# Optimization experiments

Hardware: AMD Instinct MI355X
Metric: run time of the kernel (lower is better)

Reference implementation:

```python
import jax, jax.numpy as jnp
import numpy as np

NUM_HEADS = 8

def setup_inputs() -> dict:
    key = jax.random.key(0)
    ks = jax.random.split(key, 4)
    S, B, E, ENC = 2048, 4, 512, 32
    def xavier(k, shape):
        fan_in, fan_out = shape[1], shape[0]
        lim = float(np.sqrt(6.0 / (fan_in + fan_out)))
        return jax.random.uniform(k, shape, jnp.float32, -lim, lim)
    return {
        "query": jax.random.normal(ks[0], (S, B, E), jnp.float32),
        "in_proj_weight": xavier(ks[1], (2 * ENC, E)),
        "in_proj_bias": jnp.zeros((2 * ENC,), jnp.float32),
        "v_proj_weight": xavier(ks[2], (E, E)),
        "v_proj_bias": jnp.zeros((E,), jnp.float32),
        "out_proj_weight": xavier(ks[3], (E, E)),
        "out_proj_bias": jnp.zeros((E,), jnp.float32),
    }

def reference(query, in_proj_weight, in_proj_bias, v_proj_weight, v_proj_bias,
              out_proj_weight, out_proj_bias):
    S, B, E = query.shape
    H = NUM_HEADS
    qk = query @ in_proj_weight.T + in_proj_bias          # [S, B, 2*ENC]
    q, k = jnp.split(qk, 2, axis=-1)                      # [S, B, ENC] each
    v = query @ v_proj_weight.T + v_proj_bias             # [S, B, E]
    ENC = q.shape[-1]
    dq = ENC // H   # q/k head dim (small, e.g. 4)
    dv = E // H     # v head dim (e.g. 64)
    scaling = dq ** -0.5
    # [S,B,H,d] -> [B,H,S,d]; torch's view(S, B*H, d) flattens b-major, h-minor
    q = (q * scaling).reshape(S, B, H, dq).transpose(1, 2, 0, 3)
    k = k.reshape(S, B, H, dq).transpose(1, 2, 0, 3)
    v = v.reshape(S, B, H, dv).transpose(1, 2, 0, 3)
    scores = jnp.einsum('bhsd,bhtd->bhst', q, k)          # [B,H,S,S]
    attn = jax.nn.softmax(scores, axis=-1)
    out = jnp.einsum('bhst,bhtd->bhsd', attn, v)          # [B,H,S,dv]
    out = out.transpose(2, 0, 1, 3).reshape(S, B, E)
    out = out @ out_proj_weight.T + out_proj_bias
    avg_weights = attn.sum(axis=1) / H                    # [B,S,S]
    return out, avg_weights
```

## Files before the change

### kernel.cpp

```cpp
#include <hip/hip_runtime.h>
#include <hip/hip_bf16.h>

#define S_LEN 2048
#define B_SZ 4
#define E_DIM 512
#define H_NUM 8
#define DQ 4
#define DV 64

typedef __attribute__((ext_vector_type(8))) short s16x8;
typedef __attribute__((ext_vector_type(4))) float f32x4;
typedef unsigned short u16;

__device__ __forceinline__ u16 f2b(float x) {
    __hip_bfloat16 h = __float2bfloat16(x);
    return *(u16*)&h;
}

__global__ __launch_bounds__(256) void cast_bf16(
    const float* __restrict__ q,  u16* __restrict__ qb,
    const float* __restrict__ w1, u16* __restrict__ w1b,
    const float* __restrict__ w2, u16* __restrict__ w2b,
    const float* __restrict__ w3, u16* __restrict__ w3b)
{
    const int NQ = S_LEN * B_SZ * E_DIM / 8;
    const int N1 = 64 * E_DIM / 8;
    const int N2 = E_DIM * E_DIM / 8;
    const int total = NQ + N1 + 2 * N2;
    for (int g = blockIdx.x * 256 + threadIdx.x; g < total; g += gridDim.x * 256) {
        const float* src; u16* dst; int off;
        if (g < NQ)                { src = q;  dst = qb;  off = g; }
        else if (g < NQ + N1)      { src = w1; dst = w1b; off = g - NQ; }
        else if (g < NQ + N1 + N2) { src = w2; dst = w2b; off = g - NQ - N1; }
        else                       { src = w3; dst = w3b; off = g - NQ - N1 - N2; }
        float4 a = ((const float4*)src)[(size_t)off * 2];
        float4 b = ((const float4*)src)[(size_t)off * 2 + 1];
        s16x8 o;
        o[0] = f2b(a.x); o[1] = f2b(a.y); o[2] = f2b(a.z); o[3] = f2b(a.w);
        o[4] = f2b(b.x); o[5] = f2b(b.y); o[6] = f2b(b.z); o[7] = f2b(b.w);
        ((s16x8*)dst)[off] = o;
    }
}

template <int MODE>
__global__ __launch_bounds__(256) void gemm_mfma(
    const u16* __restrict__ Abf,
    const u16* __restrict__ W1, const float* __restrict__ b1,
    const u16* __restrict__ W2, const float* __restrict__ b2,
    float* __restrict__ C,
    float* __restrict__ qs, float* __restrict__ ks,
    u16* __restrict__ vsb,
    int N, int K)
{
    constexpr int PP = 72;
    __shared__ __align__(16) u16 As[128][PP];
    __shared__ __align__(16) u16 Bs[64][PP];

    const int m0 = blockIdx.x * 128;
    const int n0 = blockIdx.y * 64;
    const int tid = threadIdx.x;
    const int w = tid >> 6, lane = tid & 63;
    const int wm = w >> 1, wn = w & 1;
    const int fr = lane & 15;
    const int fk = (lane >> 4) << 3;

    const u16* Wsel; int nbase;
    if (MODE == 0 || n0 < 64) { Wsel = W1; nbase = n0; }
    else                      { Wsel = W2; nbase = n0 - 64; }

    const int ar = tid >> 1, ah = (tid & 1) << 5;
    const int br = tid >> 2, bq = (tid & 3) << 4;

    f32x4 acc[4][2];
#pragma unroll
    for (int mt = 0; mt < 4; ++mt)
#pragma unroll
        for (int nt = 0; nt < 2; ++nt) acc[mt][nt] = (f32x4){0.f, 0.f, 0.f, 0.f};

    for (int kp = 0; kp < K; kp += 64) {
        const s16x8* ap = (const s16x8*)&Abf[(size_t)(m0 + ar) * K + kp + ah];
        s16x8 a0 = ap[0], a1 = ap[1], a2 = ap[2], a3 = ap[3];
        const s16x8* bp = (const s16x8*)&Wsel[(size_t)(nbase + br) * K + kp + bq];
        s16x8 b0 = bp[0], b1v = bp[1];
        __syncthreads();
        *(s16x8*)&As[ar][ah + 0]  = a0;
        *(s16x8*)&As[ar][ah + 8]  = a1;
        *(s16x8*)&As[ar][ah + 16] = a2;
        *(s16x8*)&As[ar][ah + 24] = a3;
        *(s16x8*)&Bs[br][bq + 0]  = b0;
        *(s16x8*)&Bs[br][bq + 8]  = b1v;
        __syncthreads();

#pragma unroll
        for (int kb = 0; kb < 2; ++kb) {
            s16x8 bf0 = *(const s16x8*)&Bs[wn * 32 + fr][(kb << 5) + fk];
            s16x8 bf1 = *(const s16x8*)&Bs[wn * 32 + 16 + fr][(kb << 5) + fk];
#pragma unroll
            for (int mt = 0; mt < 4; ++mt) {
                s16x8 af = *(const s16x8*)&As[wm * 64 + mt * 16 + fr][(kb << 5) + fk];
                acc[mt][0] = __builtin_amdgcn_mfma_f32_16x16x32_bf16(af, bf0, acc[mt][0], 0, 0, 0);
                acc[mt][1] = __builtin_amdgcn_mfma_f32_16x16x32_bf16(af, bf1, acc[mt][1], 0, 0, 0);
            }
        }
    }

#pragma unroll
    for (int mt = 0; mt < 4; ++mt)
#pragma unroll
        for (int nt = 0; nt < 2; ++nt)
#pragma unroll
            for (int j = 0; j < 4; ++j) {
                int m = m0 + wm * 64 + mt * 16 + ((lane >> 4) << 2) + j;
                int c = n0 + wn * 32 + nt * 16 + fr;
                float val = acc[mt][nt][j];
                if (MODE == 0) {
                    C[(size_t)m * N + c] = val + b1[c];
                } else {
                    int s  = m >> 2;
                    int bb = m & 3;
                    if (c < 64) {
                        val += b1[c];
                        if (c < 32) {
                            qs[((((size_t)bb * H_NUM) + (c >> 2)) * S_LEN + s) * DQ + (c & 3)] = val * 0.5f;
                        } else {
                            int j2 = c - 32;
                            ks[((((size_t)bb * H_NUM) + (j2 >> 2)) * S_LEN + s) * DQ + (j2 & 3)] = val;
                        }
                    } else {
                        int j2 = c - 64;
                        val += b2[j2];
                        vsb[((((size_t)bb * H_NUM) + (j2 >> 6)) * S_LEN + s) * DV + (j2 & 63)] = f2b(val);
                    }
                }
            }
}

__global__ __launch_bounds__(256) void lsum_kernel(
    const float* __restrict__ qs, const float* __restrict__ ks,
    float* __restrict__ linv)
{
    const int bh = blockIdx.x;
    const int s0 = blockIdx.y * 64;
    const int sl = threadIdx.x >> 2;
    const int tq = threadIdx.x & 3;
    __shared__ float Ksm[S_LEN][DQ];
    __shared__ float part[64][4];
    const float* kp = ks + (size_t)bh * S_LEN * DQ;
    for (int i = threadIdx.x; i < S_LEN; i += 256)
        *(float4*)&Ksm[i][0] = *(const float4*)&kp[(size_t)i * DQ];
    __syncthreads();

    const float4 q = *(const float4*)&qs[((size_t)bh * S_LEN + s0 + sl) * DQ];
    float l = 0.f;
    const int t0 = tq * (S_LEN / 4);
#pragma unroll 4
    for (int t = t0; t < t0 + S_LEN / 4; ++t) {
        float4 kk = *(const float4*)&Ksm[t][0];
        float sc = q.x * kk.x + q.y * kk.y + q.z * kk.z + q.w * kk.w;
        l += __expf(sc);
    }
    part[sl][tq] = l;
    __syncthreads();
    if (threadIdx.x < 64) {
        float tsum = part[threadIdx.x][0] + part[threadIdx.x][1] +
                     part[threadIdx.x][2] + part[threadIdx.x][3];
        linv[(size_t)bh * S_LEN + s0 + threadIdx.x] = 1.0f / tsum;
    }
}

__global__ __launch_bounds__(512) void attn_fused(
    const float* __restrict__ qs, const float* __restrict__ ks,
    const u16* __restrict__ vsb, const float* __restrict__ linv,
    float* __restrict__ aw, u16* __restrict__ ao)
{
    constexpr int TQ = 32, TT = 64, PP = 72;
    const int b = blockIdx.x;
    const int s0 = blockIdx.y * TQ;
    const int tid = threadIdx.x;
    const int w = tid >> 6;
    const int lane = tid & 63;

    __shared__ float Kc[H_NUM][TT][DQ];
    __shared__ float qt[H_NUM][TQ][DQ];
    __shared__ float linvs[H_NUM][TQ];
    __shared__ __align__(16) u16 pb[H_NUM][TQ][PP];
    __shared__ __align__(16) u16 vt[H_NUM][DV][PP];

    if (tid < 256) {
        int h = tid >> 5, s = tid & 31;
        *(float4*)&qt[h][s][0] =
            *(const float4*)&qs[((((size_t)b * H_NUM) + h) * S_LEN + s0 + s) * DQ];
        linvs[h][s] = linv[(((size_t)b * H_NUM) + h) * S_LEN + s0 + s];
    }

    f32x4 acc[2][4];
#pragma unroll
    for (int m = 0; m < 2; ++m)
#pragma unroll
        for (int n = 0; n < 4; ++n) acc[m][n] = (f32x4){0.f, 0.f, 0.f, 0.f};

    const u16* vb = vsb + (((size_t)b * H_NUM) + w) * S_LEN * DV;
    const float* krow = ks + (((size_t)b * H_NUM) + w) * S_LEN * DQ;
    float* awrow = aw + ((size_t)b * S_LEN + s0) * S_LEN;

    const int fr = lane & 15;
    const int fk = (lane >> 4) << 3;

    for (int t0 = 0; t0 < S_LEN; t0 += TT) {
        __syncthreads();

        *(float4*)&Kc[w][lane][0] = *(const float4*)&krow[(size_t)(t0 + lane) * DQ];
        {
            const u16* vrow = vb + (size_t)(t0 + lane) * DV;
#pragma unroll
            for (int g = 0; g < 8; ++g) {
                s16x8 vv = *(const s16x8*)(vrow + (g << 3));
#pragma unroll
                for (int j = 0; j < 8; ++j)
                    vt[w][(g << 3) + j][lane] = (u16)vv[j];
            }
        }
        __syncthreads();

        float awacc[4] = {0.f, 0.f, 0.f, 0.f};
        for (int h = 0; h < H_NUM; ++h) {
            float4 kk = *(const float4*)&Kc[h][lane][0];
#pragma unroll
            for (int it = 0; it < 4; ++it) {
                int s = w + (it << 3);
                float4 q = *(const float4*)&qt[h][s][0];
                float sc = q.x * kk.x + q.y * kk.y + q.z * kk.z + q.w * kk.w;
                float p = __expf(sc) * linvs[h][s];
                pb[h][s][lane] = f2b(p);
                awacc[it] += p;
            }
        }
#pragma unroll
        for (int it = 0; it < 4; ++it)
            awrow[(size_t)(w + (it << 3)) * S_LEN + t0 + lane] = awacc[it] * 0.125f;

        __syncthreads();

#pragma unroll
        for (int kb = 0; kb < 2; ++kb) {
            s16x8 a0 = *(const s16x8*)&pb[w][fr][(kb << 5) + fk];
            s16x8 a1 = *(const s16x8*)&pb[w][16 + fr][(kb << 5) + fk];
#pragma unroll
            for (int n = 0; n < 4; ++n) {
                s16x8 bb = *(const s16x8*)&vt[w][(n << 4) + fr][(kb << 5) + fk];
                acc[0][n] = __builtin_amdgcn_mfma_f32_16x16x32_bf16(a0, bb, acc[0][n], 0, 0, 0);
                acc[1][n] = __builtin_amdgcn_mfma_f32_16x16x32_bf16(a1, bb, acc[1][n], 0, 0, 0);
            }
        }
    }

#pragma unroll
    for (int m = 0; m < 2; ++m)
#pragma unroll
        for (int n = 0; n < 4; ++n)
#pragma unroll
            for (int j = 0; j < 4; ++j) {
                int s = (m << 4) + ((lane >> 4) << 2) + j;
                int d = (n << 4) + (lane & 15);
                ao[((size_t)(s0 + s) * B_SZ + b) * E_DIM + (w * DV + d)] =
                    f2b(acc[m][n][j]);
            }
}

extern "C" void kernel_launch(void* const* d_in, const int* in_sizes, int n_in,
                              void* d_out, int out_size, void* d_ws, size_t ws_size,
                              hipStream_t stream) {
    const float* query = (const float*)d_in[0];
    const float* ipw   = (const float*)d_in[1];
    const float* ipb   = (const float*)d_in[2];
    const float* vpw   = (const float*)d_in[3];
    const float* vpb   = (const float*)d_in[4];
    const float* opw   = (const float*)d_in[5];
    const float* opb   = (const float*)d_in[6];

    float* out_main = (float*)d_out;
    float* aw       = (float*)d_out + (size_t)S_LEN * B_SZ * E_DIM;

    const size_t NQKV = (size_t)B_SZ * H_NUM * S_LEN;
    float* qs   = (float*)d_ws;
    float* ks   = qs + NQKV * DQ;
    float* linv = ks + NQKV * DQ;
    u16* vsb    = (u16*)(linv + NQKV);
    u16* qbf    = vsb + (size_t)S_LEN * B_SZ * E_DIM;
    u16* aobf   = qbf;
    u16* ipwbf  = qbf + (size_t)S_LEN * B_SZ * E_DIM;
    u16* vpwbf  = ipwbf + 64 * E_DIM;
    u16* opwbf  = vpwbf + (size_t)E_DIM * E_DIM;

    cast_bf16<<<1024, 256, 0, stream>>>(query, qbf, ipw, ipwbf, vpw, vpwbf, opw, opwbf);

    dim3 g1(8192 / 128, 576 / 64);
    gemm_mfma<1><<<g1, 256, 0, stream>>>(qbf, ipwbf, ipb, vpwbf, vpb,
                                         nullptr, qs, ks, vsb, 576, E_DIM);

    lsum_kernel<<<dim3(B_SZ * H_NUM, S_LEN / 64), 256, 0, stream>>>(qs, ks, linv);

    attn_fused<<<dim3(B_SZ, S_LEN / 32), 512, 0, stream>>>(qs, ks, vsb, linv, aw, aobf);

    dim3 g4(8192 / 128, 512 / 64);
    gemm_mfma<0><<<g4, 256, 0, stream>>>(aobf, opwbf, opb, nullptr, nullptr,
                                         out_main, nullptr, nullptr, nullptr, E_DIM, E_DIM);
}
```

Baseline: 328.5 us.

## Store V transposed in global memory and recompute probabilities in MFMA fragments

The QKV projection now writes V transposed ([b,h,d,s]), so the attention kernel loads V tiles with vector copies instead of a scalar per-element transpose into shared memory. The bf16 probability tile in shared memory is gone. Each wave recomputes the exp scores for its own head directly into its MFMA A fragments, which removes one barrier per tile. The costs are duplicated exp work and strided 2-byte scatter stores in the GEMM epilogue when writing transposed V.

Result: slower. 362.6 us (+10.4%).

```diff
diff --git a/kernel.cpp b/kernel.cpp
--- a/kernel.cpp
+++ b/kernel.cpp
@@ -49,7 +49,7 @@
     const u16* __restrict__ W2, const float* __restrict__ b2,
     float* __restrict__ C,
     float* __restrict__ qs, float* __restrict__ ks,
-    u16* __restrict__ vsb,
+    u16* __restrict__ vtg,
     int N, int K)
 {
     constexpr int PP = 72;
@@ -129,7 +129,7 @@
                     } else {
                         int j2 = c - 64;
                         val += b2[j2];
-                        vsb[((((size_t)bb * H_NUM) + (j2 >> 6)) * S_LEN + s) * DV + (j2 & 63)] = f2b(val);
+                        vtg[((((size_t)bb * H_NUM) + (j2 >> 6)) * DV + (j2 & 63)) * S_LEN + s] = f2b(val);
                     }
                 }
             }
@@ -170,7 +170,7 @@
 
 __global__ __launch_bounds__(512) void attn_fused(
     const float* __restrict__ qs, const float* __restrict__ ks,
-    const u16* __restrict__ vsb, const float* __restrict__ linv,
+    const u16* __restrict__ vtg, const float* __restrict__ linv,
     float* __restrict__ aw, u16* __restrict__ ao)
 {
     constexpr int TQ = 32, TT = 64, PP = 72;
@@ -183,7 +183,6 @@
     __shared__ float Kc[H_NUM][TT][DQ];
     __shared__ float qt[H_NUM][TQ][DQ];
     __shared__ float linvs[H_NUM][TQ];
-    __shared__ __align__(16) u16 pb[H_NUM][TQ][PP];
     __shared__ __align__(16) u16 vt[H_NUM][DV][PP];
 
     if (tid < 256) {
@@ -192,59 +191,67 @@
             *(const float4*)&qs[((((size_t)b * H_NUM) + h) * S_LEN + s0 + s) * DQ];
         linvs[h][s] = linv[(((size_t)b * H_NUM) + h) * S_LEN + s0 + s];
     }
-
-    f32x4 acc[2][4];
-#pragma unroll
-    for (int m = 0; m < 2; ++m)
-#pragma unroll
-        for (int n = 0; n < 4; ++n) acc[m][n] = (f32x4){0.f, 0.f, 0.f, 0.f};
-
-    const u16* vb = vsb + (((size_t)b * H_NUM) + w) * S_LEN * DV;
-    const float* krow = ks + (((size_t)b * H_NUM) + w) * S_LEN * DQ;
-    float* awrow = aw + ((size_t)b * S_LEN + s0) * S_LEN;
+    __syncthreads();
 
     const int fr = lane & 15;
     const int fk = (lane >> 4) << 3;
 
+    float lr[H_NUM][4];
+#pragma unroll
+    for (int h = 0; h < H_NUM; ++h)
+#pragma unroll
+        for (int it = 0; it < 4; ++it) lr[h][it] = linvs[h][w + (it << 3)];
+    float4 qA0 = *(const float4*)&qt[w][fr][0];
+    float4 qA1 = *(const float4*)&qt[w][16 + fr][0];
+    float lv0 = linvs[w][fr], lv1 = linvs[w][16 + fr];
+
+    f32x4 acc[2][4];
+#pragma unroll
+    for (int m = 0; m < 2; ++m)
+#pragma unroll
+        for (int n = 0; n < 4; ++n) acc[m][n] = (f32x4){0.f, 0.f, 0.f, 0.f};
+
+    const float* krow = ks + (((size_t)b * H_NUM) + w) * S_LEN * DQ;
+    const u16* vrow = vtg + ((((size_t)b * H_NUM) + w) * DV + lane) * S_LEN;
+    float* awrow = aw + ((size_t)b * S_LEN + s0) * S_LEN;
+
     for (int t0 = 0; t0 < S_LEN; t0 += TT) {
         __syncthreads();
 
         *(float4*)&Kc[w][lane][0] = *(const float4*)&krow[(size_t)(t0 + lane) * DQ];
-        {
-            const u16* vrow = vb + (size_t)(t0 + lane) * DV;
-#pragma unroll
-            for (int g = 0; g < 8; ++g) {
-                s16x8 vv = *(const s16x8*)(vrow + (g << 3));
-#pragma unroll
-                for (int j = 0; j < 8; ++j)
-                    vt[w][(g << 3) + j][lane] = (u16)vv[j];
-            }
+#pragma unroll
+        for (int i = 0; i < 8; ++i) {
+            s16x8 vv = *(const s16x8*)(vrow + t0 + (i << 3));
+            *(s16x8*)&vt[w][lane][i << 3] = vv;
         }
         __syncthreads();
 
         float awacc[4] = {0.f, 0.f, 0.f, 0.f};
+#pragma unroll 2
         for (int h = 0; h < H_NUM; ++h) {
             float4 kk = *(const float4*)&Kc[h][lane][0];
 #pragma unroll
             for (int it = 0; it < 4; ++it) {
-                int s = w + (it << 3);
-                float4 q = *(const float4*)&qt[h][s][0];
+                float4 q = *(const float4*)&qt[h][w + (it << 3)][0];
                 float sc = q.x * kk.x + q.y * kk.y + q.z * kk.z + q.w * kk.w;
-                float p = __expf(sc) * linvs[h][s];
-                pb[h][s][lane] = f2b(p);
-                awacc[it] += p;
+                awacc[it] += __expf(sc) * lr[h][it];
             }
         }
 #pragma unroll
         for (int it = 0; it < 4; ++it)
             awrow[(size_t)(w + (it << 3)) * S_LEN + t0 + lane] = awacc[it] * 0.125f;
 
-        __syncthreads();
-
 #pragma unroll
         for (int kb = 0; kb < 2; ++kb) {
-            s16x8 a0 = *(const s16x8*)&pb[w][fr][(kb << 5) + fk];
-            s16x8 a1 = *(const s16x8*)&pb[w][16 + fr][(kb << 5) + fk];
+            s16x8 a0, a1;
+#pragma unroll
+            for (int j = 0; j < 8; ++j) {
+                float4 kk = *(const float4*)&Kc[w][(kb << 5) + fk + j][0];
+                float sc0 = qA0.x * kk.x + qA0.y * kk.y + qA0.z * kk.z + qA0.w * kk.w;
+                float sc1 = qA1.x * kk.x + qA1.y * kk.y + qA1.z * kk.z + qA1.w * kk.w;
+                a0[j] = (short)f2b(__expf(sc0) * lv0);
+                a1[j] = (short)f2b(__expf(sc1) * lv1);
+            }
 #pragma unroll
             for (int n = 0; n < 4; ++n) {
                 s16x8 bb = *(const s16x8*)&vt[w][(n << 4) + fr][(kb << 5) + fk];
@@ -261,7 +268,7 @@
 #pragma unroll
             for (int j = 0; j < 4; ++j) {
                 int s = (m << 4) + ((lane >> 4) << 2) + j;
-                int d = (n << 4) + (lane & 15);
+                int d = (n << 4) + fr;
                 ao[((size_t)(s0 + s) * B_SZ + b) * E_DIM + (w * DV + d)] =
                     f2b(acc[m][n][j]);
             }
@@ -285,8 +292,8 @@
     float* qs   = (float*)d_ws;
     float* ks   = qs + NQKV * DQ;
     float* linv = ks + NQKV * DQ;
-    u16* vsb    = (u16*)(linv + NQKV);
-    u16* qbf    = vsb + (size_t)S_LEN * B_SZ * E_DIM;
+    u16* vtg    = (u16*)(linv + NQKV);
+    u16* qbf    = vtg + (size_t)S_LEN * B_SZ * E_DIM;
     u16* aobf   = qbf;
     u16* ipwbf  = qbf + (size_t)S_LEN * B_SZ * E_DIM;
     u16* vpwbf  = ipwbf + 64 * E_DIM;
@@ -296,11 +303,11 @@
 
     dim3 g1(8192 / 128, 576 / 64);
     gemm_mfma<1><<<g1, 256, 0, stream>>>(qbf, ipwbf, ipb, vpwbf, vpb,
-                                         nullptr, qs, ks, vsb, 576, E_DIM);
+                                         nullptr, qs, ks, vtg, 576, E_DIM);
 
     lsum_kernel<<<dim3(B_SZ * H_NUM, S_LEN / 64), 256, 0, stream>>>(qs, ks, linv);
 
-    attn_fused<<<dim3(B_SZ, S_LEN / 32), 512, 0, stream>>>(qs, ks, vsb, linv, aw, aobf);
+    attn_fused<<<dim3(B_SZ, S_LEN / 32), 512, 0, stream>>>(qs, ks, vtg, linv, aw, aobf);
 
     dim3 g4(8192 / 128, 512 / 64);
     gemm_mfma<0><<<g4, 256, 0, stream>>>(aobf, opwbf, opb, nullptr, nullptr,
```
